# Optimization experiments

Measured on AMD Instinct MI355X. Metric: run time of the kernel, lower is better.

Reference implementation:

```python
import jax, jax.numpy as jnp
import numpy as np

N_L, N_N = 50000, 50000
E = 600000
G = 64
D = 128
LN_EPS = 1e-5


def _ln(x, g, b):
    mu = jnp.mean(x, axis=-1, keepdims=True)
    var = jnp.mean((x - mu) ** 2, axis=-1, keepdims=True)
    return (x - mu) * jax.lax.rsqrt(var + LN_EPS) * g + b


def _gconv(x_src, W, b, src, dst, n_src, n_dst):
    # DGL GraphConv, norm='both': D_dst^{-1/2} A D_src^{-1/2} X W + b
    ones = jnp.ones((src.shape[0],), x_src.dtype)
    deg_out = jnp.maximum(jax.ops.segment_sum(ones, src, num_segments=n_src), 1.0)
    deg_in = jnp.maximum(jax.ops.segment_sum(ones, dst, num_segments=n_dst), 1.0)
    xs = (x_src * jax.lax.rsqrt(deg_out)[:, None]) @ W   # project first (in>=out)
    agg = jax.ops.segment_sum(xs[src], dst, num_segments=n_dst)
    return agg * jax.lax.rsqrt(deg_in)[:, None] + b


def _seg_mean(x, gid, g):
    s = jax.ops.segment_sum(x, gid, num_segments=g)
    c = jax.ops.segment_sum(jnp.ones((x.shape[0],), x.dtype), gid, num_segments=g)
    return s / jnp.maximum(c, 1.0)[:, None]


def setup_inputs() -> dict:
    key = jax.random.key(0)
    ks = jax.random.split(key, 16)
    s = 0.05
    return {
        "feat_l": jax.random.normal(ks[0], (N_L, 300), jnp.float32),
        "feat_n": jax.random.normal(ks[1], (N_N, 200), jnp.float32),
        "W0_l2n": jax.random.normal(ks[2], (300, D), jnp.float32) * s,
        "b0_l2n": jnp.zeros((D,), jnp.float32),
        "W0_n2l": jax.random.normal(ks[3], (200, D), jnp.float32) * s,
        "b0_n2l": jnp.zeros((D,), jnp.float32),
        "W_l2n": jax.random.normal(ks[4], (2, D, D), jnp.float32) * s,
        "b_l2n": jnp.zeros((2, D), jnp.float32),
        "W_n2l": jax.random.normal(ks[5], (2, D, D), jnp.float32) * s,
        "b_n2l": jnp.zeros((2, D), jnp.float32),
        "ln_g_n": jnp.ones((3, D), jnp.float32),
        "ln_b_n": jnp.zeros((3, D), jnp.float32),
        "ln_g_l": jnp.ones((3, D), jnp.float32),
        "ln_b_l": jnp.zeros((3, D), jnp.float32),
        "W_fc": jax.random.normal(ks[6], (D, D), jnp.float32) * s,
        "b_fc": jnp.zeros((D,), jnp.float32),
        "W_out": jax.random.normal(ks[7], (D, 1), jnp.float32) * s,
        "b_out": jnp.zeros((1,), jnp.float32),
        "src_l2n": jax.random.randint(ks[8], (E,), 0, N_L, jnp.int32),
        "dst_l2n": jax.random.randint(ks[9], (E,), 0, N_N, jnp.int32),
        "src_n2l": jax.random.randint(ks[10], (E,), 0, N_N, jnp.int32),
        "dst_n2l": jax.random.randint(ks[11], (E,), 0, N_L, jnp.int32),
        "gid_l": jnp.sort(jax.random.randint(ks[12], (N_L,), 0, G, jnp.int32)),
        "gid_n": jnp.sort(jax.random.randint(ks[13], (N_N,), 0, G, jnp.int32)),
        "num_graphs": G,
    }


def reference(feat_l, feat_n, W0_l2n, b0_l2n, W0_n2l, b0_n2l,
              W_l2n, b_l2n, W_n2l, b_n2l,
              ln_g_n, ln_b_n, ln_g_l, ln_b_l,
              W_fc, b_fc, W_out, b_out,
              src_l2n, dst_l2n, src_n2l, dst_n2l, gid_l, gid_n, num_graphs):
    Ws_l2n = [W0_l2n, W_l2n[0], W_l2n[1]]
    bs_l2n = [b0_l2n, b_l2n[0], b_l2n[1]]
    Ws_n2l = [W0_n2l, W_n2l[0], W_n2l[1]]
    bs_n2l = [b0_n2l, b_n2l[0], b_n2l[1]]
    h_l, h_n = feat_l, feat_n
    n_l, n_n = feat_l.shape[0], feat_n.shape[0]
    for i in range(3):
        new_n = _gconv(h_l, Ws_l2n[i], bs_l2n[i], src_l2n, dst_l2n, n_l, n_n)
        new_l = _gconv(h_n, Ws_n2l[i], bs_n2l[i], src_n2l, dst_n2l, n_n, n_l)
        h_n = jax.nn.elu(_ln(new_n, ln_g_n[i], ln_b_n[i]))
        h_l = jax.nn.elu(_ln(new_l, ln_g_l[i], ln_b_l[i]))
    hg = _seg_mean(h_l, gid_l, num_graphs) + _seg_mean(h_n, gid_n, num_graphs)
    hg = jax.nn.relu(hg @ W_fc + b_fc)
    return hg @ W_out + b_out
```

## Files before the change

kernel.cpp:

```cpp
#include <hip/hip_runtime.h>
#include <math.h>

#define NL 50000
#define NN 50000
#define NE 600000
#define NG 64
#define DD 128
#define MPAD 50048
#define PSPLIT 8
#define MAXDEG 64

typedef unsigned short u16;
typedef unsigned int u32;
using bf16x8 = __attribute__((ext_vector_type(8))) short;
using f32x4  = __attribute__((ext_vector_type(4))) float;

__device__ __forceinline__ u16 f2bf(float x) {
    u32 u = __float_as_uint(x);
    u32 r = (u + 0x7fffu + ((u >> 16) & 1u)) >> 16;
    return (u16)r;
}
__device__ __forceinline__ float bf2f(u16 x) {
    return __uint_as_float(((u32)x) << 16);
}
__device__ __forceinline__ void gload16(const void* g, void* l) {
    __builtin_amdgcn_global_load_lds((const __attribute__((address_space(1))) void*)g,
                                     (__attribute__((address_space(3))) void*)l, 16, 0, 0);
}
__device__ __forceinline__ u32 cvtpk(float lo, float hi) {
    u32 r;
    asm("v_cvt_pk_bf16_f32 %0, %1, %2" : "=v"(r) : "v"(lo), "v"(hi));
    return r;
}

__global__ __launch_bounds__(256) void deg_ell(const int* __restrict__ s0a, const int* __restrict__ d0a,
                                               int* __restrict__ hs0, int* __restrict__ hd0,
                                               u16* __restrict__ ell0,
                                               const int* __restrict__ s1a, const int* __restrict__ d1a,
                                               int* __restrict__ hs1, int* __restrict__ hd1,
                                               u16* __restrict__ ell1, int E) {
    int e = blockIdx.x * blockDim.x + threadIdx.x;
    if (e >= E) return;
    int s0 = s0a[e], d0 = d0a[e];
    int s1 = s1a[e], d1 = d1a[e];
    atomicAdd(&hs0[s0], 1);
    atomicAdd(&hs1[s1], 1);
    int p0 = atomicAdd(&hd0[d0], 1);
    int p1 = atomicAdd(&hd1[d1], 1);
    if (p0 < MAXDEG) ell0[(size_t)d0 * MAXDEG + p0] = (u16)s0;
    if (p1 < MAXDEG) ell1[(size_t)d1 * MAXDEG + p1] = (u16)s1;
}

__global__ void rsq_kernel(const int* __restrict__ cnt, float* __restrict__ out, int n) {
    int i = blockIdx.x * blockDim.x + threadIdx.x;
    if (i < n) out[i] = rsqrtf(fmaxf((float)cnt[i], 1.0f));
}

struct ConvArgs {
    const float* W[6];
    u16* Wt[6];
    int K[6];
    int KP[6];
    int boff[7];
};
__global__ __launch_bounds__(256) void conv_all(ConvArgs a) {
    int b = blockIdx.x;
    int s = 0;
    while (s < 5 && b >= a.boff[s + 1]) ++s;
    int i = (b - a.boff[s]) * 256 + threadIdx.x;
    int KP = a.KP[s];
    if (i >= 128 * KP) return;
    int n = i / KP, k = i % KP;
    float v = (k < a.K[s]) ? a.W[s][(size_t)k * 128 + n] : 0.0f;
    a.Wt[s][i] = f2bf(v);
}

template<int KP>
__global__ __launch_bounds__(256) void mfma_gemm0(const float* __restrict__ A, int K, int M,
                                                  const u16* __restrict__ Wt,
                                                  const float* __restrict__ rsq,
                                                  u16* __restrict__ out) {
    constexpr int NT = KP / 32;
    __shared__ __align__(16) u16 As[2][64 * 32];
    __shared__ __align__(16) u16 Bs[2][128 * 32];
    const int t    = threadIdx.x;
    const int lane = t & 63;
    const int wid  = t >> 6;
    const int wr   = wid >> 1;
    const int wc   = wid & 1;
    const int brow = blockIdx.x * 64;
    const int l15  = lane & 15;
    const int kg   = lane >> 4;

    f32x4 acc[2][4];
#pragma unroll
    for (int mi = 0; mi < 2; ++mi)
#pragma unroll
        for (int ni = 0; ni < 4; ++ni) acc[mi][ni] = (f32x4){0.f, 0.f, 0.f, 0.f};

    const int ar   = t >> 2;
    const int ac   = t & 3;
    const int akey = (ar >> 1) & 3;
    const int grow = brow + ar;
    const int bn0 = t >> 2;
    const int bn1 = (256 + t) >> 2;
    const u16* b_src0 = Wt + (size_t)bn0 * KP + ((t & 3) ^ ((bn0 >> 1) & 3)) * 8;
    const u16* b_src1 = Wt + (size_t)bn1 * KP + ((t & 3) ^ ((bn1 >> 1) & 3)) * 8;

#define STAGE_B(kt, buf)                                                          \
    do {                                                                          \
        gload16(b_src0 + (kt) * 32, (char*)&Bs[buf][0] + wid * 1024);             \
        gload16(b_src1 + (kt) * 32, (char*)&Bs[buf][0] + 4096 + wid * 1024);      \
    } while (0)

    struct A8 { float4 x, y; };
    auto loadA = [&](int kt) -> A8 {
        int kbase = kt * 32 + (ac ^ akey) * 8;
        const float* p = A + (size_t)grow * K + kbase;
        A8 r;
        bool rowok = grow < M;
        r.x = (rowok && kbase + 4 <= K) ? *(const float4*)p       : make_float4(0.f, 0.f, 0.f, 0.f);
        r.y = (rowok && kbase + 8 <= K) ? *(const float4*)(p + 4) : make_float4(0.f, 0.f, 0.f, 0.f);
        return r;
    };
    auto writeA = [&](int buf, const A8& r) {
        uint4 w = make_uint4(cvtpk(r.x.x, r.x.y), cvtpk(r.x.z, r.x.w),
                             cvtpk(r.y.x, r.y.y), cvtpk(r.y.z, r.y.w));
        *(uint4*)&As[buf][ar * 32 + ac * 8] = w;
    };

    A8 rnext{};
    {
        A8 r0 = loadA(0);
        if (NT > 1) rnext = loadA(1);
        writeA(0, r0);
        STAGE_B(0, 0);
    }
    __syncthreads();

    const int fo = (kg ^ ((l15 >> 1) & 3)) * 8;
#pragma unroll
    for (int kt = 0; kt < NT; ++kt) {
        const int cur = kt & 1;
        if (kt + 1 < NT) {
            writeA(cur ^ 1, rnext);
            STAGE_B(kt + 1, cur ^ 1);
            if (kt + 2 < NT) rnext = loadA(kt + 2);
        }
        bf16x8 a0 = *(const bf16x8*)&As[cur][(wr * 32 +  0 + l15) * 32 + fo];
        bf16x8 a1 = *(const bf16x8*)&As[cur][(wr * 32 + 16 + l15) * 32 + fo];
#pragma unroll
        for (int ni = 0; ni < 4; ++ni) {
            bf16x8 b = *(const bf16x8*)&Bs[cur][(wc * 64 + ni * 16 + l15) * 32 + fo];
            acc[0][ni] = __builtin_amdgcn_mfma_f32_16x16x32_bf16(a0, b, acc[0][ni], 0, 0, 0);
            acc[1][ni] = __builtin_amdgcn_mfma_f32_16x16x32_bf16(a1, b, acc[1][ni], 0, 0, 0);
        }
        __syncthreads();
    }
#undef STAGE_B

#pragma unroll
    for (int mi = 0; mi < 2; ++mi)
#pragma unroll
        for (int r = 0; r < 4; ++r) {
            int go = brow + wr * 32 + mi * 16 + kg * 4 + r;
            if (go < M) {
                float s = rsq[go];
#pragma unroll
                for (int ni = 0; ni < 4; ++ni)
                    out[(size_t)go * 128 + wc * 64 + ni * 16 + l15] = f2bf(acc[mi][ni][r] * s);
            }
        }
}

struct MDir {
    const u16* agg; const float* rsq_dst; const u16* Wt;
    const float* bias; const float* gw; const float* bln; u16* out;
};
__global__ __launch_bounds__(256) void gemm128_ln(MDir da, MDir db, int M, int nblk) {
    __shared__ __align__(16) u16 Bs[128 * 128];
    __shared__ __align__(16) u16 As[64 * 128];
    __shared__ float rs[2][64][2];
    const MDir& d = ((int)blockIdx.x < nblk) ? da : db;
    const int bid = ((int)blockIdx.x < nblk) ? blockIdx.x : blockIdx.x - nblk;
    const int base = bid * 64;
    const int t    = threadIdx.x;
    const int lane = t & 63;
    const int wid  = t >> 6;
    const int wr   = wid >> 1;
    const int wc   = wid & 1;
    const int l15  = lane & 15;
    const int kg   = lane >> 4;

#pragma unroll
    for (int j = 0; j < 8; ++j) {
        int lidx = j * 256 + t;
        int n = lidx >> 4, p = lidx & 15;
        int lg = (p >> 2) ^ (n & 3);
        int lc = (p & 3) ^ ((n >> 2) & 3);
        const u16* src = d.Wt + (size_t)n * 128 + (lg * 4 + lc) * 8;
        void* dst = (char*)Bs + (size_t)(j * 256 + (t & ~63)) * 16;
        gload16(src, dst);
    }
#pragma unroll
    for (int j = 0; j < 4; ++j) {
        int lidx = j * 256 + t;
        int row = lidx >> 4, p = lidx & 15;
        int lg = (p >> 2) ^ (row & 3);
        int lc = (p & 3) ^ ((row >> 2) & 3);
        const u16* src = d.agg + (size_t)(base + row) * 128 + (lg * 4 + lc) * 8;
        void* dst = (char*)As + (size_t)(j * 256 + (t & ~63)) * 16;
        gload16(src, dst);
    }
    float b4[4], g4[4], bl4[4];
#pragma unroll
    for (int ni = 0; ni < 4; ++ni) {
        int c = wc * 64 + ni * 16 + l15;
        b4[ni] = d.bias[c]; g4[ni] = d.gw[c]; bl4[ni] = d.bln[c];
    }
    __syncthreads();

    const int key1r = l15 & 3;
    const int key2r = (l15 >> 2) & 3;
    f32x4 acc[2][4];
#pragma unroll
    for (int mi = 0; mi < 2; ++mi)
#pragma unroll
        for (int ni = 0; ni < 4; ++ni) acc[mi][ni] = (f32x4){0.f, 0.f, 0.f, 0.f};
#pragma unroll
    for (int kt = 0; kt < 4; ++kt) {
        int pA = (((kt ^ key1r) * 4) + (kg ^ key2r)) * 8;
        bf16x8 a0 = *(const bf16x8*)&As[(size_t)(wr * 32 +  0 + l15) * 128 + pA];
        bf16x8 a1 = *(const bf16x8*)&As[(size_t)(wr * 32 + 16 + l15) * 128 + pA];
#pragma unroll
        for (int ni = 0; ni < 4; ++ni) {
            bf16x8 b = *(const bf16x8*)&Bs[(size_t)(wc * 64 + ni * 16 + l15) * 128 + pA];
            acc[0][ni] = __builtin_amdgcn_mfma_f32_16x16x32_bf16(a0, b, acc[0][ni], 0, 0, 0);
            acc[1][ni] = __builtin_amdgcn_mfma_f32_16x16x32_bf16(a1, b, acc[1][ni], 0, 0, 0);
        }
    }

    float rsv[2][4];
#pragma unroll
    for (int mi = 0; mi < 2; ++mi)
#pragma unroll
        for (int r = 0; r < 4; ++r) {
            int go = base + wr * 32 + mi * 16 + kg * 4 + r;
            rsv[mi][r] = (go < M) ? d.rsq_dst[go] : 0.0f;
        }
#pragma unroll
    for (int mi = 0; mi < 2; ++mi)
#pragma unroll
        for (int r = 0; r < 4; ++r) {
            int lrow = wr * 32 + mi * 16 + kg * 4 + r;
            float s1 = 0.f, s2 = 0.f;
#pragma unroll
            for (int ni = 0; ni < 4; ++ni) {
                float xv = acc[mi][ni][r] * rsv[mi][r] + b4[ni];
                s1 += xv; s2 += xv * xv;
            }
#pragma unroll
            for (int m = 1; m < 16; m <<= 1) {
                s1 += __shfl_xor(s1, m, 64);
                s2 += __shfl_xor(s2, m, 64);
            }
            if (l15 == 0) { rs[0][lrow][wc] = s1; rs[1][lrow][wc] = s2; }
        }
    __syncthreads();
#pragma unroll
    for (int mi = 0; mi < 2; ++mi)
#pragma unroll
        for (int r = 0; r < 4; ++r) {
            int lrow = wr * 32 + mi * 16 + kg * 4 + r;
            int go = base + lrow;
            if (go < M) {
                float S1 = rs[0][lrow][0] + rs[0][lrow][1];
                float S2 = rs[1][lrow][0] + rs[1][lrow][1];
                float mu = S1 * (1.0f / 128.0f);
                float var = S2 * (1.0f / 128.0f) - mu * mu;
                float rstd = rsqrtf(fmaxf(var, 0.0f) + 1e-5f);
#pragma unroll
                for (int ni = 0; ni < 4; ++ni) {
                    float xv = acc[mi][ni][r] * rsv[mi][r] + b4[ni];
                    float y = (xv - mu) * rstd * g4[ni] + bl4[ni];
                    y = (y > 0.0f) ? y : expm1f(y);
                    d.out[(size_t)go * 128 + wc * 64 + ni * 16 + l15] = f2bf(y);
                }
            }
        }
}

struct GDir {
    const u16* xs; const u16* ell; const int* cnt; const float* rsq_in;
    const float* bias; const float* g; const float* bln; u16* out;
};
__global__ __launch_bounds__(256) void gather_ln2(GDir da, GDir db, int M, int nblk) {
    const GDir& d = ((int)blockIdx.x < nblk) ? da : db;
    const int bid = ((int)blockIdx.x < nblk) ? blockIdx.x : blockIdx.x - nblk;
    int row  = bid * 4 + (threadIdx.x >> 6);
    int lane = threadIdx.x & 63;
    int grp  = lane >> 4;
    int i16  = lane & 15;
    if (row >= M) return;
    int n = min(d.cnt[row], MAXDEG);
    const u16* col = d.ell + (size_t)row * MAXDEG;

    float acc[8];
#pragma unroll
    for (int k = 0; k < 8; ++k) acc[k] = 0.f;
    for (int e = grp; e < n; e += 4) {
        int s = col[e];
        uint4 v = *(const uint4*)&d.xs[(size_t)s * 128 + i16 * 8];
        acc[0] += bf2f((u16)v.x); acc[1] += bf2f((u16)(v.x >> 16));
        acc[2] += bf2f((u16)v.y); acc[3] += bf2f((u16)(v.y >> 16));
        acc[4] += bf2f((u16)v.z); acc[5] += bf2f((u16)(v.z >> 16));
        acc[6] += bf2f((u16)v.w); acc[7] += bf2f((u16)(v.w >> 16));
    }
#pragma unroll
    for (int k = 0; k < 8; ++k) {
        acc[k] += __shfl_xor(acc[k], 16, 64);
        acc[k] += __shfl_xor(acc[k], 32, 64);
    }

    float sc = d.rsq_in[row];
    float4 bva = *(const float4*)&d.bias[i16 * 8];
    float4 bvb = *(const float4*)&d.bias[i16 * 8 + 4];
    float x[8];
    x[0] = acc[0] * sc + bva.x; x[1] = acc[1] * sc + bva.y;
    x[2] = acc[2] * sc + bva.z; x[3] = acc[3] * sc + bva.w;
    x[4] = acc[4] * sc + bvb.x; x[5] = acc[5] * sc + bvb.y;
    x[6] = acc[6] * sc + bvb.z; x[7] = acc[7] * sc + bvb.w;

    float s1 = 0.f, s2 = 0.f;
#pragma unroll
    for (int k = 0; k < 8; ++k) { s1 += x[k]; s2 += x[k] * x[k]; }
#pragma unroll
    for (int m = 1; m < 16; m <<= 1) {
        s1 += __shfl_xor(s1, m, 64);
        s2 += __shfl_xor(s2, m, 64);
    }
    float mu = s1 * (1.0f / 128.0f);
    float var = s2 * (1.0f / 128.0f) - mu * mu;
    float rstd = rsqrtf(fmaxf(var, 0.0f) + 1e-5f);

    if (grp == 0) {
        float4 gva = *(const float4*)&d.g[i16 * 8];
        float4 gvb = *(const float4*)&d.g[i16 * 8 + 4];
        float4 lba = *(const float4*)&d.bln[i16 * 8];
        float4 lbb = *(const float4*)&d.bln[i16 * 8 + 4];
        float gv[8] = {gva.x, gva.y, gva.z, gva.w, gvb.x, gvb.y, gvb.z, gvb.w};
        float lb[8] = {lba.x, lba.y, lba.z, lba.w, lbb.x, lbb.y, lbb.z, lbb.w};
        float y[8];
#pragma unroll
        for (int k = 0; k < 8; ++k) {
            float tv = (x[k] - mu) * rstd * gv[k] + lb[k];
            y[k] = (tv > 0.0f) ? tv : expm1f(tv);
        }
        uint4 o = make_uint4(cvtpk(y[0], y[1]), cvtpk(y[2], y[3]),
                             cvtpk(y[4], y[5]), cvtpk(y[6], y[7]));
        *(uint4*)&d.out[(size_t)row * 128 + i16 * 8] = o;
    }
}

struct SDir {
    const u16* h; const u16* ell; const int* cnt; const float* rsq_src; u16* agg;
};
__global__ __launch_bounds__(256) void gather_scale2(SDir da, SDir db, int M, int nblk) {
    const SDir& d = ((int)blockIdx.x < nblk) ? da : db;
    const int bid = ((int)blockIdx.x < nblk) ? blockIdx.x : blockIdx.x - nblk;
    int row  = bid * 4 + (threadIdx.x >> 6);
    int lane = threadIdx.x & 63;
    int grp  = lane >> 4;
    int i16  = lane & 15;
    if (row >= M) return;
    int n = min(d.cnt[row], MAXDEG);
    const u16* col = d.ell + (size_t)row * MAXDEG;

    float acc[8];
#pragma unroll
    for (int k = 0; k < 8; ++k) acc[k] = 0.f;
    for (int e = grp; e < n; e += 4) {
        int s = col[e];
        float r = d.rsq_src[s];
        uint4 v = *(const uint4*)&d.h[(size_t)s * 128 + i16 * 8];
        acc[0] = fmaf(r, bf2f((u16)v.x), acc[0]); acc[1] = fmaf(r, bf2f((u16)(v.x >> 16)), acc[1]);
        acc[2] = fmaf(r, bf2f((u16)v.y), acc[2]); acc[3] = fmaf(r, bf2f((u16)(v.y >> 16)), acc[3]);
        acc[4] = fmaf(r, bf2f((u16)v.z), acc[4]); acc[5] = fmaf(r, bf2f((u16)(v.z >> 16)), acc[5]);
        acc[6] = fmaf(r, bf2f((u16)v.w), acc[6]); acc[7] = fmaf(r, bf2f((u16)(v.w >> 16)), acc[7]);
    }
#pragma unroll
    for (int k = 0; k < 8; ++k) {
        acc[k] += __shfl_xor(acc[k], 16, 64);
        acc[k] += __shfl_xor(acc[k], 32, 64);
    }
    if (grp == 0) {
        uint4 o = make_uint4(cvtpk(acc[0], acc[1]), cvtpk(acc[2], acc[3]),
                             cvtpk(acc[4], acc[5]), cvtpk(acc[6], acc[7]));
        *(uint4*)&d.agg[(size_t)row * 128 + i16 * 8] = o;
    }
}

struct PDir { const u16* h; const int* gid; float* partial; };
__global__ __launch_bounds__(128) void pool2(PDir da, PDir db, int M, int nblk) {
    const PDir& d = ((int)blockIdx.x < nblk) ? da : db;
    const int bid = ((int)blockIdx.x < nblk) ? blockIdx.x : blockIdx.x - nblk;
    int g = bid / PSPLIT;
    int p = bid % PSPLIT;
    int j = threadIdx.x;
    int f  = j & 63;
    int rh = j >> 6;
    __shared__ int bounds[2];
    if (j < 2) {
        int target = g + j;
        int lo = 0, hi = M;
        while (lo < hi) { int mid = (lo + hi) >> 1; if (d.gid[mid] < target) lo = mid + 1; else hi = mid; }
        bounds[j] = lo;
    }
    __syncthreads();
    int beg = bounds[0], end = bounds[1];
    int len = end - beg;
    int chunk = (len + PSPLIT - 1) / PSPLIT;
    int s0i = beg + p * chunk;
    int e0i = min(s0i + chunk, end);
    const u32* h32 = (const u32*)d.h;

    float a0 = 0.f, a1 = 0.f, b0 = 0.f, b1 = 0.f;
    int i = s0i + rh;
    for (; i + 2 < e0i; i += 4) {
        u32 v0 = h32[(size_t)i * 64 + f];
        u32 v1 = h32[(size_t)(i + 2) * 64 + f];
        a0 += bf2f((u16)v0); a1 += bf2f((u16)(v0 >> 16));
        b0 += bf2f((u16)v1); b1 += bf2f((u16)(v1 >> 16));
    }
    if (i < e0i) {
        u32 v = h32[(size_t)i * 64 + f];
        a0 += bf2f((u16)v); a1 += bf2f((u16)(v >> 16));
    }
    float2 o = make_float2(a0 + b0, a1 + b1);
    *(float2*)&d.partial[((size_t)(g * PSPLIT + p) * 2 + rh) * 128 + f * 2] = o;
}

__global__ __launch_bounds__(128) void head_kernel(const float* __restrict__ part_l,
                                                   const float* __restrict__ part_n,
                                                   const int* __restrict__ gid_l,
                                                   const int* __restrict__ gid_n,
                                                   const float* __restrict__ W_fc,
                                                   const float* __restrict__ b_fc,
                                                   const float* __restrict__ W_out,
                                                   const float* __restrict__ b_out,
                                                   float* __restrict__ out) {
    int g = blockIdx.x;
    int j = threadIdx.x;
    __shared__ float hg[128];
    __shared__ float red[2];
    __shared__ int bounds[4];
    if (j < 4) {
        const int* gid = (j < 2) ? gid_l : gid_n;
        int target = g + (j & 1);
        int lo = 0, hi = 50000;
        while (lo < hi) { int mid = (lo + hi) >> 1; if (gid[mid] < target) lo = mid + 1; else hi = mid; }
        bounds[j] = lo;
    }
    __syncthreads();
    float cl = fmaxf((float)(bounds[1] - bounds[0]), 1.0f);
    float cn = fmaxf((float)(bounds[3] - bounds[2]), 1.0f);
    float sl = 0.f, sn = 0.f;
#pragma unroll
    for (int q = 0; q < 2 * PSPLIT; ++q) {
        sl += part_l[((size_t)g * 2 * PSPLIT + q) * 128 + j];
        sn += part_n[((size_t)g * 2 * PSPLIT + q) * 128 + j];
    }
    hg[j] = sl / cl + sn / cn;
    __syncthreads();
    float acc = b_fc[j];
#pragma unroll 8
    for (int k = 0; k < 128; ++k) acc = fmaf(hg[k], W_fc[k * 128 + j], acc);
    float fc = fmaxf(acc, 0.0f);
    float v = fc * W_out[j];
#pragma unroll
    for (int m = 1; m < 64; m <<= 1) v += __shfl_xor(v, m, 64);
    if ((j & 63) == 0) red[j >> 6] = v;
    __syncthreads();
    if (j == 0) out[g] = red[0] + red[1] + b_out[0];
}

static inline size_t align_up(size_t x, size_t a) { return (x + a - 1) & ~(a - 1); }

extern "C" void kernel_launch(void* const* d_in, const int* in_sizes, int n_in,
                              void* d_out, int out_size, void* d_ws, size_t ws_size,
                              hipStream_t stream) {
    const float* feat_l = (const float*)d_in[0];
    const float* feat_n = (const float*)d_in[1];
    const float* W0_l2n = (const float*)d_in[2];
    const float* b0_l2n = (const float*)d_in[3];
    const float* W0_n2l = (const float*)d_in[4];
    const float* b0_n2l = (const float*)d_in[5];
    const float* W_l2n  = (const float*)d_in[6];
    const float* b_l2n  = (const float*)d_in[7];
    const float* W_n2l  = (const float*)d_in[8];
    const float* b_n2l  = (const float*)d_in[9];
    const float* ln_g_n = (const float*)d_in[10];
    const float* ln_b_n = (const float*)d_in[11];
    const float* ln_g_l = (const float*)d_in[12];
    const float* ln_b_l = (const float*)d_in[13];
    const float* W_fc   = (const float*)d_in[14];
    const float* b_fc   = (const float*)d_in[15];
    const float* W_out  = (const float*)d_in[16];
    const float* b_out  = (const float*)d_in[17];
    const int* src_l2n  = (const int*)d_in[18];
    const int* dst_l2n  = (const int*)d_in[19];
    const int* src_n2l  = (const int*)d_in[20];
    const int* dst_n2l  = (const int*)d_in[21];
    const int* gid_l    = (const int*)d_in[22];
    const int* gid_n    = (const int*)d_in[23];

    char* ws = (char*)d_ws;
    size_t off = 0;
    auto take = [&](size_t bytes) { char* p = ws + off; off = align_up(off + bytes, 256); return p; };
    int*   icnt        = (int*)take(200000 * 4);
    float* rsq         = (float*)take(200000 * 4);
    u16*   ell_l2n     = (u16*)take((size_t)NN * MAXDEG * 2);
    u16*   ell_n2l     = (u16*)take((size_t)NL * MAXDEG * 2);
    u16*   Wt0_l2n     = (u16*)take(128 * 320 * 2);
    u16*   Wt0_n2l     = (u16*)take(128 * 224 * 2);
    u16*   Wt_l2n0     = (u16*)take(128 * 128 * 2);
    u16*   Wt_l2n1     = (u16*)take(128 * 128 * 2);
    u16*   Wt_n2l0     = (u16*)take(128 * 128 * 2);
    u16*   Wt_n2l1     = (u16*)take(128 * 128 * 2);
    u16*   buf0        = (u16*)take((size_t)MPAD * 128 * 2);
    u16*   buf1        = (u16*)take((size_t)MPAD * 128 * 2);
    u16*   buf2        = (u16*)take((size_t)MPAD * 128 * 2);
    u16*   buf3        = (u16*)take((size_t)MPAD * 128 * 2);
    float* part_l      = (float*)take((size_t)NG * PSPLIT * 2 * 128 * 4);
    float* part_n      = (float*)take((size_t)NG * PSPLIT * 2 * 128 * 4);

    int* icnt_src_l2n = icnt;
    int* icnt_dst_l2n = icnt + NL;
    int* icnt_src_n2l = icnt + NL + NN;
    int* icnt_dst_n2l = icnt + NL + 2 * NN;
    float* rsq_src_l2n = rsq;
    float* rsq_dst_l2n = rsq + NL;
    float* rsq_src_n2l = rsq + NL + NN;
    float* rsq_dst_n2l = rsq + NL + 2 * NN;

    const int TB = 256;
    const int gemm_grid = MPAD / 64;
    const int gath_grid = (NL + 3) / 4;
    const int edge_grid = (NE + TB - 1) / TB;

    hipMemsetAsync(icnt, 0, 200000 * sizeof(int), stream);
    deg_ell<<<edge_grid, TB, 0, stream>>>(src_l2n, dst_l2n, icnt_src_l2n, icnt_dst_l2n, ell_l2n,
                                          src_n2l, dst_n2l, icnt_src_n2l, icnt_dst_n2l, ell_n2l, NE);
    rsq_kernel<<<(200000 + TB - 1) / TB, TB, 0, stream>>>(icnt, rsq, 200000);

    {
        ConvArgs a;
        a.W[0] = W0_l2n;            a.Wt[0] = Wt0_l2n; a.K[0] = 300; a.KP[0] = 320;
        a.W[1] = W0_n2l;            a.Wt[1] = Wt0_n2l; a.K[1] = 200; a.KP[1] = 224;
        a.W[2] = W_l2n;             a.Wt[2] = Wt_l2n0; a.K[2] = 128; a.KP[2] = 128;
        a.W[3] = W_l2n + 128 * 128; a.Wt[3] = Wt_l2n1; a.K[3] = 128; a.KP[3] = 128;
        a.W[4] = W_n2l;             a.Wt[4] = Wt_n2l0; a.K[4] = 128; a.KP[4] = 128;
        a.W[5] = W_n2l + 128 * 128; a.Wt[5] = Wt_n2l1; a.K[5] = 128; a.KP[5] = 128;
        int bo = 0;
        for (int s = 0; s < 6; ++s) { a.boff[s] = bo; bo += (128 * a.KP[s]) / 256; }
        a.boff[6] = bo;
        conv_all<<<bo, TB, 0, stream>>>(a);
    }

    u16* xs0 = buf0;
    u16* xs1 = buf1;
    u16* hn  = buf2;
    u16* hl  = buf3;
    mfma_gemm0<320><<<gemm_grid, TB, 0, stream>>>(feat_l, 300, NL, Wt0_l2n, rsq_src_l2n, xs0);
    mfma_gemm0<224><<<gemm_grid, TB, 0, stream>>>(feat_n, 200, NN, Wt0_n2l, rsq_src_n2l, xs1);
    {
        GDir ga = {xs0, ell_l2n, icnt_dst_l2n, rsq_dst_l2n, b0_l2n, ln_g_n, ln_b_n, hn};
        GDir gb = {xs1, ell_n2l, icnt_dst_n2l, rsq_dst_n2l, b0_n2l, ln_g_l, ln_b_l, hl};
        gather_ln2<<<2 * gath_grid, TB, 0, stream>>>(ga, gb, NL, gath_grid);
    }

    const u16* Wls[2] = {Wt_l2n0, Wt_l2n1};
    const u16* Wns[2] = {Wt_n2l0, Wt_n2l1};
    for (int i = 1; i <= 2; ++i) {
        const float* bl = b_l2n + (size_t)(i - 1) * DD;
        const float* bn = b_n2l + (size_t)(i - 1) * DD;
        SDir sa = {hl, ell_l2n, icnt_dst_l2n, rsq_src_l2n, buf0};
        SDir sb = {hn, ell_n2l, icnt_dst_n2l, rsq_src_n2l, buf1};
        gather_scale2<<<2 * gath_grid, TB, 0, stream>>>(sa, sb, NL, gath_grid);
        MDir ma = {buf0, rsq_dst_l2n, Wls[i - 1], bl,
                   ln_g_n + (size_t)i * DD, ln_b_n + (size_t)i * DD, hn};
        MDir mb = {buf1, rsq_dst_n2l, Wns[i - 1], bn,
                   ln_g_l + (size_t)i * DD, ln_b_l + (size_t)i * DD, hl};
        gemm128_ln<<<2 * gemm_grid, TB, 0, stream>>>(ma, mb, NL, gemm_grid);
    }

    {
        PDir pa = {hl, gid_l, part_l};
        PDir pb = {hn, gid_n, part_n};
        pool2<<<2 * NG * PSPLIT, 128, 0, stream>>>(pa, pb, NL, NG * PSPLIT);
    }
    head_kernel<<<NG, 128, 0, stream>>>(part_l, part_n, gid_l, gid_n,
                                        W_fc, b_fc, W_out, b_out, (float*)d_out);
}
```

Measured before the change: 415.9 us.

## Fuse first-layer GEMMs with degree/ELL build into one kernel

Merges the two layer-0 projection GEMMs and the edge degree-count/ELL construction kernel into a single launch, dispatching on block index so the GEMM blocks and atomic edge blocks run concurrently. To remove the GEMM's dependency on source degrees, the rsqrt(deg_out) scaling moves from the GEMM epilogue into the first gather, which now reads a per-source scale for every edge. This saves two kernel launches and lets the memory-bound atomic work overlap with compute. The cost is an extra scattered scale load per edge in the gather and a larger shared-memory footprint for the atomic blocks.

```diff
diff --git a/kernel.cpp b/kernel.cpp
--- a/kernel.cpp
+++ b/kernel.cpp
@@ -31,24 +31,6 @@
     u32 r;
     asm("v_cvt_pk_bf16_f32 %0, %1, %2" : "=v"(r) : "v"(lo), "v"(hi));
     return r;
-}
-
-__global__ __launch_bounds__(256) void deg_ell(const int* __restrict__ s0a, const int* __restrict__ d0a,
-                                               int* __restrict__ hs0, int* __restrict__ hd0,
-                                               u16* __restrict__ ell0,
-                                               const int* __restrict__ s1a, const int* __restrict__ d1a,
-                                               int* __restrict__ hs1, int* __restrict__ hd1,
-                                               u16* __restrict__ ell1, int E) {
-    int e = blockIdx.x * blockDim.x + threadIdx.x;
-    if (e >= E) return;
-    int s0 = s0a[e], d0 = d0a[e];
-    int s1 = s1a[e], d1 = d1a[e];
-    atomicAdd(&hs0[s0], 1);
-    atomicAdd(&hs1[s1], 1);
-    int p0 = atomicAdd(&hd0[d0], 1);
-    int p1 = atomicAdd(&hd1[d1], 1);
-    if (p0 < MAXDEG) ell0[(size_t)d0 * MAXDEG + p0] = (u16)s0;
-    if (p1 < MAXDEG) ell1[(size_t)d1 * MAXDEG + p1] = (u16)s1;
 }
 
 __global__ void rsq_kernel(const int* __restrict__ cnt, float* __restrict__ out, int n) {
@@ -76,19 +58,18 @@
 }
 
 template<int KP>
-__global__ __launch_bounds__(256) void mfma_gemm0(const float* __restrict__ A, int K, int M,
-                                                  const u16* __restrict__ Wt,
-                                                  const float* __restrict__ rsq,
-                                                  u16* __restrict__ out) {
+__device__ __forceinline__ void gemm0_body(int bid, const float* __restrict__ A, int K, int M,
+                                           const u16* __restrict__ Wt,
+                                           u16* __restrict__ out, char* smem) {
     constexpr int NT = KP / 32;
-    __shared__ __align__(16) u16 As[2][64 * 32];
-    __shared__ __align__(16) u16 Bs[2][128 * 32];
+    u16* As = (u16*)smem;
+    u16* Bs = (u16*)(smem + 8192);
     const int t    = threadIdx.x;
     const int lane = t & 63;
     const int wid  = t >> 6;
     const int wr   = wid >> 1;
     const int wc   = wid & 1;
-    const int brow = blockIdx.x * 64;
+    const int brow = bid * 64;
     const int l15  = lane & 15;
     const int kg   = lane >> 4;
 
@@ -109,8 +90,8 @@
 
 #define STAGE_B(kt, buf)                                                          \
     do {                                                                          \
-        gload16(b_src0 + (kt) * 32, (char*)&Bs[buf][0] + wid * 1024);             \
-        gload16(b_src1 + (kt) * 32, (char*)&Bs[buf][0] + 4096 + wid * 1024);      \
+        gload16(b_src0 + (kt) * 32, (char*)Bs + (buf) * 8192 + wid * 1024);       \
+        gload16(b_src1 + (kt) * 32, (char*)Bs + (buf) * 8192 + 4096 + wid * 1024);\
     } while (0)
 
     struct A8 { float4 x, y; };
@@ -126,7 +107,7 @@
     auto writeA = [&](int buf, const A8& r) {
         uint4 w = make_uint4(cvtpk(r.x.x, r.x.y), cvtpk(r.x.z, r.x.w),
                              cvtpk(r.y.x, r.y.y), cvtpk(r.y.z, r.y.w));
-        *(uint4*)&As[buf][ar * 32 + ac * 8] = w;
+        *(uint4*)&As[buf * 2048 + ar * 32 + ac * 8] = w;
     };
 
     A8 rnext{};
@@ -147,11 +128,11 @@
             STAGE_B(kt + 1, cur ^ 1);
             if (kt + 2 < NT) rnext = loadA(kt + 2);
         }
-        bf16x8 a0 = *(const bf16x8*)&As[cur][(wr * 32 +  0 + l15) * 32 + fo];
-        bf16x8 a1 = *(const bf16x8*)&As[cur][(wr * 32 + 16 + l15) * 32 + fo];
+        bf16x8 a0 = *(const bf16x8*)&As[cur * 2048 + (wr * 32 +  0 + l15) * 32 + fo];
+        bf16x8 a1 = *(const bf16x8*)&As[cur * 2048 + (wr * 32 + 16 + l15) * 32 + fo];
 #pragma unroll
         for (int ni = 0; ni < 4; ++ni) {
-            bf16x8 b = *(const bf16x8*)&Bs[cur][(wc * 64 + ni * 16 + l15) * 32 + fo];
+            bf16x8 b = *(const bf16x8*)&Bs[cur * 4096 + (wc * 64 + ni * 16 + l15) * 32 + fo];
             acc[0][ni] = __builtin_amdgcn_mfma_f32_16x16x32_bf16(a0, b, acc[0][ni], 0, 0, 0);
             acc[1][ni] = __builtin_amdgcn_mfma_f32_16x16x32_bf16(a1, b, acc[1][ni], 0, 0, 0);
         }
@@ -165,12 +146,43 @@
         for (int r = 0; r < 4; ++r) {
             int go = brow + wr * 32 + mi * 16 + kg * 4 + r;
             if (go < M) {
-                float s = rsq[go];
 #pragma unroll
                 for (int ni = 0; ni < 4; ++ni)
-                    out[(size_t)go * 128 + wc * 64 + ni * 16 + l15] = f2bf(acc[mi][ni][r] * s);
+                    out[(size_t)go * 128 + wc * 64 + ni * 16 + l15] = f2bf(acc[mi][ni][r]);
             }
         }
+}
+
+__global__ __launch_bounds__(256) void mega(const float* __restrict__ feat_l,
+                                            const float* __restrict__ feat_n,
+                                            const u16* __restrict__ Wt0_l2n,
+                                            const u16* __restrict__ Wt0_n2l,
+                                            u16* __restrict__ xs0, u16* __restrict__ xs1,
+                                            const int* __restrict__ s0a, const int* __restrict__ d0a,
+                                            int* __restrict__ hs0, int* __restrict__ hd0,
+                                            u16* __restrict__ ell0,
+                                            const int* __restrict__ s1a, const int* __restrict__ d1a,
+                                            int* __restrict__ hs1, int* __restrict__ hd1,
+                                            u16* __restrict__ ell1,
+                                            int gblk, int E) {
+    __shared__ __align__(16) char smem[24576];
+    int b = blockIdx.x;
+    if (b < gblk) {
+        gemm0_body<320>(b, feat_l, 300, NL, Wt0_l2n, xs0, smem);
+    } else if (b < 2 * gblk) {
+        gemm0_body<224>(b - gblk, feat_n, 200, NN, Wt0_n2l, xs1, smem);
+    } else {
+        int e = (b - 2 * gblk) * 256 + threadIdx.x;
+        if (e >= E) return;
+        int s0 = s0a[e], d0 = d0a[e];
+        int s1 = s1a[e], d1 = d1a[e];
+        atomicAdd(&hs0[s0], 1);
+        atomicAdd(&hs1[s1], 1);
+        int p0 = atomicAdd(&hd0[d0], 1);
+        int p1 = atomicAdd(&hd1[d1], 1);
+        if (p0 < MAXDEG) ell0[(size_t)d0 * MAXDEG + p0] = (u16)s0;
+        if (p1 < MAXDEG) ell1[(size_t)d1 * MAXDEG + p1] = (u16)s1;
+    }
 }
 
 struct MDir {
@@ -291,8 +303,8 @@
 }
 
 struct GDir {
-    const u16* xs; const u16* ell; const int* cnt; const float* rsq_in;
-    const float* bias; const float* g; const float* bln; u16* out;
+    const u16* xs; const u16* ell; const int* cnt; const float* rsq_src;
+    const float* rsq_in; const float* bias; const float* g; const float* bln; u16* out;
 };
 __global__ __launch_bounds__(256) void gather_ln2(GDir da, GDir db, int M, int nblk) {
     const GDir& d = ((int)blockIdx.x < nblk) ? da : db;
@@ -310,11 +322,12 @@
     for (int k = 0; k < 8; ++k) acc[k] = 0.f;
     for (int e = grp; e < n; e += 4) {
         int s = col[e];
+        float r = d.rsq_src[s];
         uint4 v = *(const uint4*)&d.xs[(size_t)s * 128 + i16 * 8];
-        acc[0] += bf2f((u16)v.x); acc[1] += bf2f((u16)(v.x >> 16));
-        acc[2] += bf2f((u16)v.y); acc[3] += bf2f((u16)(v.y >> 16));
-        acc[4] += bf2f((u16)v.z); acc[5] += bf2f((u16)(v.z >> 16));
-        acc[6] += bf2f((u16)v.w); acc[7] += bf2f((u16)(v.w >> 16));
+        acc[0] = fmaf(r, bf2f((u16)v.x), acc[0]); acc[1] = fmaf(r, bf2f((u16)(v.x >> 16)), acc[1]);
+        acc[2] = fmaf(r, bf2f((u16)v.y), acc[2]); acc[3] = fmaf(r, bf2f((u16)(v.y >> 16)), acc[3]);
+        acc[4] = fmaf(r, bf2f((u16)v.z), acc[4]); acc[5] = fmaf(r, bf2f((u16)(v.z >> 16)), acc[5]);
+        acc[6] = fmaf(r, bf2f((u16)v.w), acc[6]); acc[7] = fmaf(r, bf2f((u16)(v.w >> 16)), acc[7]);
     }
 #pragma unroll
     for (int k = 0; k < 8; ++k) {
@@ -548,11 +561,6 @@
     const int gath_grid = (NL + 3) / 4;
     const int edge_grid = (NE + TB - 1) / TB;
 
-    hipMemsetAsync(icnt, 0, 200000 * sizeof(int), stream);
-    deg_ell<<<edge_grid, TB, 0, stream>>>(src_l2n, dst_l2n, icnt_src_l2n, icnt_dst_l2n, ell_l2n,
-                                          src_n2l, dst_n2l, icnt_src_n2l, icnt_dst_n2l, ell_n2l, NE);
-    rsq_kernel<<<(200000 + TB - 1) / TB, TB, 0, stream>>>(icnt, rsq, 200000);
-
     {
         ConvArgs a;
         a.W[0] = W0_l2n;            a.Wt[0] = Wt0_l2n; a.K[0] = 300; a.KP[0] = 320;
@@ -566,16 +574,24 @@
         a.boff[6] = bo;
         conv_all<<<bo, TB, 0, stream>>>(a);
     }
+    hipMemsetAsync(icnt, 0, 200000 * sizeof(int), stream);
 
     u16* xs0 = buf0;
     u16* xs1 = buf1;
     u16* hn  = buf2;
     u16* hl  = buf3;
-    mfma_gemm0<320><<<gemm_grid, TB, 0, stream>>>(feat_l, 300, NL, Wt0_l2n, rsq_src_l2n, xs0);
-    mfma_gemm0<224><<<gemm_grid, TB, 0, stream>>>(feat_n, 200, NN, Wt0_n2l, rsq_src_n2l, xs1);
+    mega<<<2 * gemm_grid + edge_grid, TB, 0, stream>>>(
+        feat_l, feat_n, Wt0_l2n, Wt0_n2l, xs0, xs1,
+        src_l2n, dst_l2n, icnt_src_l2n, icnt_dst_l2n, ell_l2n,
+        src_n2l, dst_n2l, icnt_src_n2l, icnt_dst_n2l, ell_n2l,
+        gemm_grid, NE);
+    rsq_kernel<<<(200000 + TB - 1) / TB, TB, 0, stream>>>(icnt, rsq, 200000);
+
     {
-        GDir ga = {xs0, ell_l2n, icnt_dst_l2n, rsq_dst_l2n, b0_l2n, ln_g_n, ln_b_n, hn};
-        GDir gb = {xs1, ell_n2l, icnt_dst_n2l, rsq_dst_n2l, b0_n2l, ln_g_l, ln_b_l, hl};
+        GDir ga = {xs0, ell_l2n, icnt_dst_l2n, rsq_src_l2n, rsq_dst_l2n,
+                   b0_l2n, ln_g_n, ln_b_n, hn};
+        GDir gb = {xs1, ell_n2l, icnt_dst_n2l, rsq_src_n2l, rsq_dst_n2l,
+                   b0_n2l, ln_g_l, ln_b_l, hl};
         gather_ln2<<<2 * gath_grid, TB, 0, stream>>>(ga, gb, NL, gath_grid);
     }
 
```

New measurement: 395.6 us. -4.9%, faster.
